# Optimization experiments

Measured on AMD Instinct MI355X. Metric: run time of the kernel, lower is better.

## Reference

```python
import jax, jax.numpy as jnp
import numpy as np

NEG_SLOPE = 0.2
EPS = 1e-16

def gatv2(x, edge_index, edge_attr, Wl, bl, We, att, bias):
    """PyG GATv2Conv, heads=1, share_weights=True, with edge_dim."""
    N = x.shape[0]
    h = x @ Wl + bl                      # [N, out] shared lin_l == lin_r
    src, dst = edge_index[0], edge_index[1]
    hj = h[src]                          # source (message) features [E, out]
    hi = h[dst]                          # target features [E, out]
    e = jax.nn.leaky_relu(hi + hj + edge_attr @ We, NEG_SLOPE)  # [E, out]
    score = e @ att                      # [E]
    # segment softmax over edges grouped by destination node
    smax = jax.ops.segment_max(score, dst, num_segments=N)
    ex = jnp.exp(score - smax[dst])
    denom = jax.ops.segment_sum(ex, dst, num_segments=N)
    alpha = ex / (denom[dst] + EPS)      # [E]
    out = jax.ops.segment_sum(hj * alpha[:, None], dst, num_segments=N)
    return out + bias


def setup_inputs() -> dict:
    key = jax.random.key(0)
    N, E = 50000, 800000
    D_IN, D_LAT, D_EDGE, N_ACT = 128, 128, 16, 32
    ks = jax.random.split(key, 16)
    s = 0.05
    inp = {
        "x": jax.random.normal(ks[0], (N, D_IN), jnp.float32),
        "edge_index": jax.random.randint(ks[1], (2, E), 0, N, jnp.int32),
        "edge_attr": jax.random.normal(ks[2], (E, D_EDGE), jnp.float32),
        # gnn_layer: D_IN -> D_LAT
        "Wl1": jax.random.normal(ks[3], (D_IN, D_LAT), jnp.float32) * s,
        "bl1": jnp.zeros((D_LAT,), jnp.float32),
        "We1": jax.random.normal(ks[4], (D_EDGE, D_LAT), jnp.float32) * s,
        "att1": jax.random.normal(ks[5], (D_LAT,), jnp.float32) * s,
        "bias1": jnp.zeros((D_LAT,), jnp.float32),
        # node_layer: D_LAT -> 1
        "Wl2": jax.random.normal(ks[6], (D_LAT, 1), jnp.float32) * s,
        "bl2": jnp.zeros((1,), jnp.float32),
        "We2": jax.random.normal(ks[7], (D_EDGE, 1), jnp.float32) * s,
        "att2": jax.random.normal(ks[8], (1,), jnp.float32) * s,
        "bias2": jnp.zeros((1,), jnp.float32),
        # action_layer: D_LAT -> N_ACT
        "Wl3": jax.random.normal(ks[9], (D_LAT, N_ACT), jnp.float32) * s,
        "bl3": jnp.zeros((N_ACT,), jnp.float32),
        "We3": jax.random.normal(ks[10], (D_EDGE, N_ACT), jnp.float32) * s,
        "att3": jax.random.normal(ks[11], (N_ACT,), jnp.float32) * s,
        "bias3": jnp.zeros((N_ACT,), jnp.float32),
    }
    return inp


def reference(x, edge_index, edge_attr,
              Wl1, bl1, We1, att1, bias1,
              Wl2, bl2, We2, att2, bias2,
              Wl3, bl3, We3, att3, bias3):
    latent = gatv2(x, edge_index, edge_attr, Wl1, bl1, We1, att1, bias1)          # [N, D_LAT]
    node_logits = gatv2(latent, edge_index, edge_attr, Wl2, bl2, We2, att2, bias2)[:, 0]  # [N]
    action_logits = gatv2(latent, edge_index, edge_attr, Wl3, bl3, We3, att3, bias3)      # [N, A]
    # categorical sampling with fixed key (deterministic reference)
    k1, k2 = jax.random.split(jax.random.key(42))
    node_sel = jax.random.categorical(k1, node_logits)
    node_lp = jax.nn.log_softmax(node_logits)[node_sel]
    act_logits_sel = action_logits[node_sel, :]
    action_sel = jax.random.categorical(k2, act_logits_sel)
    action_lp = jax.nn.log_softmax(act_logits_sel)[action_sel]
    return (node_sel, action_sel, node_lp + action_lp)
```

## Files before the change

kernel.cpp:

```cpp
#include <hip/hip_runtime.h>
#include <stdint.h>
#include <math.h>

#define NEG 0.2f
#define TINYF 1.1754943508222875e-38f

typedef float f4 __attribute__((ext_vector_type(4)));
typedef float f2 __attribute__((ext_vector_type(2)));

__host__ __device__ inline void threefry2x32(uint32_t k0, uint32_t k1,
                                             uint32_t x0, uint32_t x1,
                                             uint32_t* o0, uint32_t* o1) {
  uint32_t ks0 = k0, ks1 = k1, ks2 = k0 ^ k1 ^ 0x1BD11BDAu;
  x0 += ks0; x1 += ks1;
#define RR(r) { x0 += x1; x1 = (x1 << (r)) | (x1 >> (32 - (r))); x1 ^= x0; }
  RR(13) RR(15) RR(26) RR(6)
  x0 += ks1; x1 += ks2 + 1u;
  RR(17) RR(29) RR(16) RR(24)
  x0 += ks2; x1 += ks0 + 2u;
  RR(13) RR(15) RR(26) RR(6)
  x0 += ks0; x1 += ks1 + 3u;
  RR(17) RR(29) RR(16) RR(24)
  x0 += ks1; x1 += ks2 + 4u;
  RR(13) RR(15) RR(26) RR(6)
  x0 += ks2; x1 += ks0 + 5u;
#undef RR
  *o0 = x0; *o1 = x1;
}

__device__ inline float gumbel_part(uint32_t ka, uint32_t kb, uint32_t i) {
  uint32_t o0, o1;
  threefry2x32(ka, kb, 0u, i, &o0, &o1);
  uint32_t bits = o0 ^ o1;
  float f = __uint_as_float((bits >> 9) | 0x3f800000u) - 1.0f;
  float u = fmaxf(TINYF, f + TINYF);
  return -logf(-logf(u));
}

__global__ void count_kernel(const int* __restrict__ ei, int E, int* __restrict__ counts) {
  int e = blockIdx.x * blockDim.x + threadIdx.x;
  if (e < E) atomicAdd(&counts[ei[E + e]], 1);
}

#define SCB 256
__global__ __launch_bounds__(256) void scan_partial_kernel(const int* __restrict__ counts,
    int N, int chunk, int* __restrict__ bsum) {
  int b = blockIdx.x;
  int s0 = b * chunk, s1 = s0 + chunk; if (s1 > N) s1 = N;
  int tid = threadIdx.x;
  int v = 0;
  for (int i = s0 + tid; i < s1; i += 256) v += counts[i];
  __shared__ int red[256];
  red[tid] = v; __syncthreads();
  for (int s = 128; s; s >>= 1) { if (tid < s) red[tid] += red[tid + s]; __syncthreads(); }
  if (tid == 0) bsum[b] = red[0];
}

__global__ __launch_bounds__(256) void scan_offsets_kernel(const int* __restrict__ bsum,
    int* __restrict__ boff, int* __restrict__ row_start, int N) {
  int tid = threadIdx.x; int lane = tid & 63; int wv = tid >> 6;
  __shared__ int wsum[4];
  int v = bsum[tid];
  int incl = v;
#pragma unroll
  for (int off = 1; off < 64; off <<= 1) {
    int t = __shfl_up(incl, off);
    if (lane >= off) incl += t;
  }
  if (lane == 63) wsum[wv] = incl;
  __syncthreads();
  if (tid == 0) {
    int s = 0;
    for (int k = 0; k < 4; k++) { int t = wsum[k]; wsum[k] = s; s += t; }
    row_start[N] = s;
  }
  __syncthreads();
  boff[tid] = wsum[wv] + incl - v;
}

__global__ __launch_bounds__(256) void scan_apply_kernel(const int* __restrict__ counts,
    const int* __restrict__ boff, int N, int chunk,
    int* __restrict__ row_start, int* __restrict__ cursor) {
  int b = blockIdx.x;
  int s0 = b * chunk, s1 = s0 + chunk; if (s1 > N) s1 = N;
  int tid = threadIdx.x; int lane = tid & 63; int wv = tid >> 6;
  __shared__ int wsum[4];
  __shared__ int tot_s;
  __shared__ int base_s;
  if (tid == 0) base_s = boff[b];
  __syncthreads();
  for (int c0 = s0; c0 < s1; c0 += 256) {
    int i = c0 + tid;
    int v = (i < s1) ? counts[i] : 0;
    int incl = v;
#pragma unroll
    for (int off = 1; off < 64; off <<= 1) {
      int t = __shfl_up(incl, off);
      if (lane >= off) incl += t;
    }
    if (lane == 63) wsum[wv] = incl;
    __syncthreads();
    if (tid == 0) {
      int s = 0;
      for (int k = 0; k < 4; k++) { int t = wsum[k]; wsum[k] = s; s += t; }
      tot_s = s;
    }
    __syncthreads();
    int base = base_s;
    int excl = base + wsum[wv] + incl - v;
    if (i < s1) { row_start[i] = excl; cursor[i] = excl; }
    __syncthreads();
    if (tid == 0) base_s = base + tot_s;
    __syncthreads();
  }
}

__global__ void scatter_kernel(const int* __restrict__ ei, const float* __restrict__ ea,
                               int E, int* __restrict__ cursor,
                               int* __restrict__ src_csr, float* __restrict__ ea_csr) {
  int e = blockIdx.x * blockDim.x + threadIdx.x;
  if (e < E) {
    int d = ei[E + e];
    int p = atomicAdd(&cursor[d], 1);
    src_csr[p] = ei[e];
    const float4* s4 = (const float4*)&ea[(size_t)e * 16];
    float4* d4 = (float4*)&ea_csr[(size_t)p * 16];
    float4 t0 = s4[0], t1 = s4[1], t2 = s4[2], t3 = s4[3];
    d4[0] = t0; d4[1] = t1; d4[2] = t2; d4[3] = t3;
  }
}

__global__ __launch_bounds__(256) void gemm128_kernel(const float* __restrict__ X,
    const float* __restrict__ W, const float* __restrict__ bias,
    float* __restrict__ out, int M) {
  __shared__ float xs[128][33];
  int row0 = blockIdx.x * 32;
  int tid = threadIdx.x;
  for (int idx = tid; idx < 32 * 128; idx += 256) {
    int r = idx >> 7;
    int k = idx & 127;
    int row = row0 + r;
    xs[k][r] = (row < M) ? X[(size_t)row * 128 + k] : 0.0f;
  }
  __syncthreads();
  int tc = tid & 31, tr = tid >> 5;
  int c0 = tc * 4, r0 = tr * 4;
  float acc[4][4] = {};
#pragma unroll 4
  for (int k = 0; k < 128; k++) {
    float4 w = *(const float4*)&W[k * 128 + c0];
    float x0 = xs[k][r0], x1 = xs[k][r0 + 1], x2 = xs[k][r0 + 2], x3 = xs[k][r0 + 3];
    acc[0][0] += x0 * w.x; acc[0][1] += x0 * w.y; acc[0][2] += x0 * w.z; acc[0][3] += x0 * w.w;
    acc[1][0] += x1 * w.x; acc[1][1] += x1 * w.y; acc[1][2] += x1 * w.z; acc[1][3] += x1 * w.w;
    acc[2][0] += x2 * w.x; acc[2][1] += x2 * w.y; acc[2][2] += x2 * w.z; acc[2][3] += x2 * w.w;
    acc[3][0] += x3 * w.x; acc[3][1] += x3 * w.y; acc[3][2] += x3 * w.z; acc[3][3] += x3 * w.w;
  }
  float4 b4 = *(const float4*)&bias[c0];
  for (int r = 0; r < 4; r++) {
    int row = row0 + r0 + r;
    if (row < M) {
      float4 o;
      o.x = acc[r][0] + b4.x; o.y = acc[r][1] + b4.y;
      o.z = acc[r][2] + b4.z; o.w = acc[r][3] + b4.w;
      *(float4*)&out[(size_t)row * 128 + c0] = o;
    }
  }
}

__global__ __launch_bounds__(256) void gemm32_kernel(const float* __restrict__ X,
    const float* __restrict__ W, const float* __restrict__ bias,
    float* __restrict__ out, int M) {
  int t = blockIdx.x * 256 + threadIdx.x;
  int node = t >> 5, c = t & 31;
  if (node >= M) return;
  const float4* xp = (const float4*)&X[(size_t)node * 128];
  float acc = 0.f;
#pragma unroll
  for (int q = 0; q < 32; q++) {
    float4 x4 = xp[q];
    acc += x4.x * W[(q * 4 + 0) * 32 + c] + x4.y * W[(q * 4 + 1) * 32 + c]
         + x4.z * W[(q * 4 + 2) * 32 + c] + x4.w * W[(q * 4 + 3) * 32 + c];
  }
  out[(size_t)node * 32 + c] = acc + bias[c];
}

__global__ __launch_bounds__(256) void gemv_kernel(const float* __restrict__ X,
    const float* __restrict__ w, const float* __restrict__ b0,
    float* __restrict__ out, int M) {
  int wv = (blockIdx.x * 256 + threadIdx.x) >> 6;
  int lane = threadIdx.x & 63;
  if (wv >= M) return;
  float2 xv = *(const float2*)&X[(size_t)wv * 128 + lane * 2];
  float2 wvv = *(const float2*)&w[lane * 2];
  float v = xv.x * wvv.x + xv.y * wvv.y;
#pragma unroll
  for (int off = 32; off; off >>= 1) v += __shfl_xor(v, off);
  if (lane == 0) out[wv] = v + b0[0];
}

__global__ __launch_bounds__(256) void fused1_kernel(const float* __restrict__ h,
    const int* __restrict__ src_csr, const int* __restrict__ row_start,
    const float* __restrict__ ea_csr,
    const float* __restrict__ We, const float* __restrict__ att,
    const float* __restrict__ bias, float* __restrict__ out, int N) {
  __shared__ float WeS[2048];
  int tid = threadIdx.x;
  for (int i = tid; i < 2048; i += 256) WeS[i] = We[i];
  __syncthreads();
  int hw = (blockIdx.x * 256 + tid) >> 5;
  int lane = tid & 31;
  if (hw >= N) return;
  int c4 = lane * 4;
  const f4* W4 = (const f4*)WeS;
  f4 attv = *(const f4*)&att[c4];
  f4 bb = *(const f4*)&bias[c4];
  int start = row_start[hw];
  int deg = row_start[hw + 1] - start;
  if (deg == 0) {
    *(f4*)&out[(size_t)hw * 128 + c4] = bb;
    return;
  }
  f4 hi = *(const f4*)&h[(size_t)hw * 128 + c4];
  int s_l = (lane < deg) ? src_csr[start + lane] : 0;
  int dcap = deg < 32 ? deg : 32;
  const f4* eap = (const f4*)&ea_csr[(size_t)start * 16];
  float m = -INFINITY, l = 0.f;
  f4 acc = (f4)0.f;
  for (int j = 0; j < deg; j++) {
    int s = (j < dcap) ? __shfl(s_l, j, 32) : src_csr[start + j];
    f4 hj = *(const f4*)&h[(size_t)s * 128 + c4];
    f4 v = hi + hj;
#pragma unroll
    for (int q = 0; q < 4; q++) {
      f4 aq = eap[(size_t)j * 4 + q];
      v += aq.x * W4[(4 * q + 0) * 32 + lane];
      v += aq.y * W4[(4 * q + 1) * 32 + lane];
      v += aq.z * W4[(4 * q + 2) * 32 + lane];
      v += aq.w * W4[(4 * q + 3) * 32 + lane];
    }
    v.x = v.x >= 0.f ? v.x : NEG * v.x;
    v.y = v.y >= 0.f ? v.y : NEG * v.y;
    v.z = v.z >= 0.f ? v.z : NEG * v.z;
    v.w = v.w >= 0.f ? v.w : NEG * v.w;
    f4 pv = v * attv;
    float sc = (pv.x + pv.y) + (pv.z + pv.w);
#pragma unroll
    for (int off = 16; off; off >>= 1) sc += __shfl_xor(sc, off);
    float mn = fmaxf(m, sc);
    float scale = __expf(m - mn);
    float w = __expf(sc - mn);
    l = l * scale + w;
    acc = acc * scale + w * hj;
    m = mn;
  }
  float inv = 1.0f / (l + 1e-16f);
  f4 o = acc * inv + bb;
  *(f4*)&out[(size_t)hw * 128 + c4] = o;
}

__global__ __launch_bounds__(256) void fused23_kernel(
    const float* __restrict__ h3, const float* __restrict__ h2,
    const int* __restrict__ src_csr, const int* __restrict__ row_start,
    const float* __restrict__ ea_csr,
    const float* __restrict__ We3, const float* __restrict__ att3,
    const float* __restrict__ bias3, const float* __restrict__ We2,
    const float* __restrict__ att2, const float* __restrict__ bias2,
    float* __restrict__ out3, float* __restrict__ logits, int N) {
  __shared__ float We3S[512];
  __shared__ float att3S[32];
  __shared__ float We2S[16];
  int tid = threadIdx.x;
  for (int i = tid; i < 512; i += 256) We3S[i] = We3[i];
  if (tid < 32) att3S[tid] = att3[tid];
  if (tid < 16) We2S[tid] = We2[tid];
  __syncthreads();
  int wv = (blockIdx.x * 256 + tid) >> 6;
  int lane = tid & 63;
  if (wv >= N) return;
  int q4 = lane >> 4;
  int l16 = lane & 15;
  int c2 = l16 * 2;
  const f2* W3 = (const f2*)We3S;
  f2 at3 = *(const f2*)&att3S[c2];
  float a2s = att2[0];
  f2 bi3 = *(const f2*)&bias3[c2];
  int start = row_start[wv];
  int deg = row_start[wv + 1] - start;
  if (deg == 0) {
    if (lane < 16) *(f2*)&out3[(size_t)wv * 32 + c2] = bi3;
    if (lane == 0) logits[wv] = bias2[0];
    return;
  }
  f2 hi3 = *(const f2*)&h3[(size_t)wv * 32 + c2];
  float hi2 = h2[wv];
  int s_l = (lane < deg) ? src_csr[start + lane] : 0;
  int dcap = deg < 64 ? deg : 64;
  const float4* eap = (const float4*)&ea_csr[(size_t)start * 16];
  float m3 = -INFINITY, l3 = 0.f; f2 a3 = (f2)0.f;
  float m2 = -INFINITY, l2 = 0.f; float a2 = 0.f;
  for (int j = q4; j < deg; j += 4) {
    int s = (j < dcap) ? __shfl(s_l, j) : src_csr[start + j];
    f2 hj3 = *(const f2*)&h3[(size_t)s * 32 + c2];
    float h2s = h2[s];
    float4 c0 = eap[(size_t)j * 4 + 0];
    float4 c1 = eap[(size_t)j * 4 + 1];
    float4 cc2 = eap[(size_t)j * 4 + 2];
    float4 c3 = eap[(size_t)j * 4 + 3];
    f2 v = hi3 + hj3;
    v += c0.x * W3[0 * 16 + l16];  v += c0.y * W3[1 * 16 + l16];
    v += c0.z * W3[2 * 16 + l16];  v += c0.w * W3[3 * 16 + l16];
    v += c1.x * W3[4 * 16 + l16];  v += c1.y * W3[5 * 16 + l16];
    v += c1.z * W3[6 * 16 + l16];  v += c1.w * W3[7 * 16 + l16];
    v += cc2.x * W3[8 * 16 + l16]; v += cc2.y * W3[9 * 16 + l16];
    v += cc2.z * W3[10 * 16 + l16]; v += cc2.w * W3[11 * 16 + l16];
    v += c3.x * W3[12 * 16 + l16]; v += c3.y * W3[13 * 16 + l16];
    v += c3.z * W3[14 * 16 + l16]; v += c3.w * W3[15 * 16 + l16];
    v.x = v.x >= 0.f ? v.x : NEG * v.x;
    v.y = v.y >= 0.f ? v.y : NEG * v.y;
    float t3 = v.x * at3.x + v.y * at3.y;
#pragma unroll
    for (int off = 8; off; off >>= 1) t3 += __shfl_xor(t3, off);
    float v2 = hi2 + h2s;
    v2 += c0.x * We2S[0]  + c0.y * We2S[1]  + c0.z * We2S[2]  + c0.w * We2S[3];
    v2 += c1.x * We2S[4]  + c1.y * We2S[5]  + c1.z * We2S[6]  + c1.w * We2S[7];
    v2 += cc2.x * We2S[8] + cc2.y * We2S[9] + cc2.z * We2S[10] + cc2.w * We2S[11];
    v2 += c3.x * We2S[12] + c3.y * We2S[13] + c3.z * We2S[14] + c3.w * We2S[15];
    v2 = v2 >= 0.f ? v2 : NEG * v2;
    float t2 = v2 * a2s;
    float mn3 = fmaxf(m3, t3);
    float sc3 = __expf(m3 - mn3);
    float w3 = __expf(t3 - mn3);
    l3 = l3 * sc3 + w3;
    a3 = a3 * sc3 + w3 * hj3;
    m3 = mn3;
    float mn2 = fmaxf(m2, t2);
    float sc2 = __expf(m2 - mn2);
    float w2 = __expf(t2 - mn2);
    l2 = l2 * sc2 + w2;
    a2 = a2 * sc2 + w2 * h2s;
    m2 = mn2;
  }
#pragma unroll
  for (int off = 16; off <= 32; off <<= 1) {
    float m3o = __shfl_xor(m3, off), l3o = __shfl_xor(l3, off);
    float ax = __shfl_xor(a3.x, off), ay = __shfl_xor(a3.y, off);
    float M3 = fmaxf(m3, m3o);
    float sA = (m3 == -INFINITY) ? 0.f : __expf(m3 - M3);
    float sB = (m3o == -INFINITY) ? 0.f : __expf(m3o - M3);
    l3 = l3 * sA + l3o * sB;
    a3.x = a3.x * sA + ax * sB;
    a3.y = a3.y * sA + ay * sB;
    m3 = M3;
    float m2o = __shfl_xor(m2, off), l2o = __shfl_xor(l2, off);
    float az = __shfl_xor(a2, off);
    float M2 = fmaxf(m2, m2o);
    float tA = (m2 == -INFINITY) ? 0.f : __expf(m2 - M2);
    float tB = (m2o == -INFINITY) ? 0.f : __expf(m2o - M2);
    l2 = l2 * tA + l2o * tB;
    a2 = a2 * tA + az * tB;
    m2 = M2;
  }
  if (lane < 16) {
    f2 o;
    o.x = a3.x / (l3 + 1e-16f) + bi3.x;
    o.y = a3.y / (l3 + 1e-16f) + bi3.y;
    *(f2*)&out3[(size_t)wv * 32 + c2] = o;
  }
  if (lane == 0) logits[wv] = a2 / (l2 + 1e-16f) + bias2[0];
}

#define NSB 64
__global__ __launch_bounds__(256) void node_partial_kernel(const float* __restrict__ logits,
    int N, uint32_t ka, uint32_t kb,
    float* __restrict__ pB, int* __restrict__ pI,
    float* __restrict__ pM, float* __restrict__ pL) {
  int chunk = (N + NSB - 1) / NSB;
  int s0 = blockIdx.x * chunk;
  int s1 = s0 + chunk; if (s1 > N) s1 = N;
  int tid = threadIdx.x;
  float best = -INFINITY; int bi = 0x7fffffff;
  float m = -INFINITY, l = 0.f;
  for (int i = s0 + tid; i < s1; i += 256) {
    float lg = logits[i];
    float mn = fmaxf(m, lg);
    l = l * __expf(m - mn) + __expf(lg - mn);
    m = mn;
    float v = lg + gumbel_part(ka, kb, (uint32_t)i);
    if (v > best) { best = v; bi = i; }
  }
  __shared__ float sb[256], sm[256], sl[256];
  __shared__ int si[256];
  sb[tid] = best; si[tid] = bi; sm[tid] = m; sl[tid] = l;
  __syncthreads();
  for (int s = 128; s; s >>= 1) {
    if (tid < s) {
      if (sb[tid + s] > sb[tid] || (sb[tid + s] == sb[tid] && si[tid + s] < si[tid])) {
        sb[tid] = sb[tid + s]; si[tid] = si[tid + s];
      }
      float M = fmaxf(sm[tid], sm[tid + s]);
      float t0 = (sm[tid] == -INFINITY) ? 0.f : sl[tid] * __expf(sm[tid] - M);
      float t1 = (sm[tid + s] == -INFINITY) ? 0.f : sl[tid + s] * __expf(sm[tid + s] - M);
      sm[tid] = M; sl[tid] = t0 + t1;
    }
    __syncthreads();
  }
  if (tid == 0) { pB[blockIdx.x] = sb[0]; pI[blockIdx.x] = si[0]; pM[blockIdx.x] = sm[0]; pL[blockIdx.x] = sl[0]; }
}

__global__ __launch_bounds__(64) void node_final_kernel(const float* __restrict__ logits,
    const float* __restrict__ pB, const int* __restrict__ pI,
    const float* __restrict__ pM, const float* __restrict__ pL,
    float* __restrict__ scal) {
  int lane = threadIdx.x;
  float best = pB[lane]; int bi = pI[lane];
  float m = pM[lane]; float l = pL[lane];
#pragma unroll
  for (int off = 32; off; off >>= 1) {
    float ob = __shfl_xor(best, off); int oi = __shfl_xor(bi, off);
    if (ob > best || (ob == best && oi < bi)) { best = ob; bi = oi; }
    float om = __shfl_xor(m, off); float ol = __shfl_xor(l, off);
    float M = fmaxf(m, om);
    float t0 = (m == -INFINITY) ? 0.f : l * __expf(m - M);
    float t1 = (om == -INFINITY) ? 0.f : ol * __expf(om - M);
    m = M; l = t0 + t1;
  }
  if (lane == 0) {
    ((int*)scal)[0] = bi;
    scal[3] = logits[bi] - (m + logf(l));
  }
}

__global__ __launch_bounds__(64) void action_kernel(const float* __restrict__ out3,
    const float* __restrict__ scal, uint32_t ka, uint32_t kb,
    float* __restrict__ dout, int out_size) {
  int lane = threadIdx.x;
  int sel = ((const int*)scal)[0];
  float v = -INFINITY, noisy = -INFINITY;
  if (lane < 32) {
    v = out3[(size_t)sel * 32 + lane];
    noisy = v + gumbel_part(ka, kb, (uint32_t)lane);
  }
  int idx = lane;
  float nv = noisy;
#pragma unroll
  for (int off = 32; off; off >>= 1) {
    float ov = __shfl_xor(nv, off);
    int oi = __shfl_xor(idx, off);
    if (ov > nv || (ov == nv && oi < idx)) { nv = ov; idx = oi; }
  }
  float vm = v;
#pragma unroll
  for (int off = 32; off; off >>= 1) vm = fmaxf(vm, __shfl_xor(vm, off));
  float ex = (lane < 32) ? expf(v - vm) : 0.f;
#pragma unroll
  for (int off = 32; off; off >>= 1) ex += __shfl_xor(ex, off);
  float vsel = __shfl(v, idx);
  if (lane == 0) {
    float action_lp = vsel - vm - logf(ex);
    dout[0] = (float)sel;
    dout[1] = (float)idx;
    dout[2] = scal[3] + action_lp;
  }
  for (int i = 3 + lane; i < out_size; i += 64) dout[i] = 0.f;
}

extern "C" void kernel_launch(void* const* d_in, const int* in_sizes, int n_in,
                              void* d_out, int out_size, void* d_ws, size_t ws_size,
                              hipStream_t stream) {
  const float* x     = (const float*)d_in[0];
  const int*   ei    = (const int*)d_in[1];
  const float* ea    = (const float*)d_in[2];
  const float* Wl1   = (const float*)d_in[3];
  const float* bl1   = (const float*)d_in[4];
  const float* We1   = (const float*)d_in[5];
  const float* att1  = (const float*)d_in[6];
  const float* bias1 = (const float*)d_in[7];
  const float* Wl2   = (const float*)d_in[8];
  const float* bl2   = (const float*)d_in[9];
  const float* We2   = (const float*)d_in[10];
  const float* att2  = (const float*)d_in[11];
  const float* bias2 = (const float*)d_in[12];
  const float* Wl3   = (const float*)d_in[13];
  const float* bl3   = (const float*)d_in[14];
  const float* We3   = (const float*)d_in[15];
  const float* att3  = (const float*)d_in[16];
  const float* bias3 = (const float*)d_in[17];
  int N = in_sizes[0] / 128;
  int E = in_sizes[1] / 2;
  float* out = (float*)d_out;

  char* p = (char*)d_ws;
  auto alloc = [&](size_t bytes) -> char* {
    char* r = p; p += (bytes + 255) & ~(size_t)255; return r;
  };
  float* h1      = (float*)alloc((size_t)N * 128 * 4);
  float* latent  = (float*)alloc((size_t)N * 128 * 4);
  float* h3      = (float*)alloc((size_t)N * 32 * 4);
  float* h2      = (float*)alloc((size_t)N * 4);
  float* logits  = (float*)alloc((size_t)N * 4);
  float* out3    = (float*)alloc((size_t)N * 32 * 4);
  int* counts    = (int*)alloc((size_t)N * 4);
  int* row_start = (int*)alloc((size_t)(N + 1) * 4);
  int* cursor    = (int*)alloc((size_t)N * 4);
  int* src_csr   = (int*)alloc((size_t)E * 4);
  float* ea_csr  = (float*)alloc((size_t)E * 16 * 4);
  int* bsum      = (int*)alloc(SCB * 4);
  int* boff      = (int*)alloc(SCB * 4);
  float* pB      = (float*)alloc(NSB * 4);
  int*   pI      = (int*)alloc(NSB * 4);
  float* pM      = (float*)alloc(NSB * 4);
  float* pL      = (float*)alloc(NSB * 4);
  float* scal    = (float*)alloc(64);
  (void)ws_size; (void)n_in;

  uint32_t k1a, k1b, k2a, k2b;
  threefry2x32(0u, 42u, 0u, 0u, &k1a, &k1b);
  threefry2x32(0u, 42u, 0u, 1u, &k2a, &k2b);

  int chunk = (N + SCB - 1) / SCB;

  hipMemsetAsync(counts, 0, (size_t)N * 4, stream);
  count_kernel<<<(E + 255) / 256, 256, 0, stream>>>(ei, E, counts);
  scan_partial_kernel<<<SCB, 256, 0, stream>>>(counts, N, chunk, bsum);
  scan_offsets_kernel<<<1, 256, 0, stream>>>(bsum, boff, row_start, N);
  scan_apply_kernel<<<SCB, 256, 0, stream>>>(counts, boff, N, chunk, row_start, cursor);
  scatter_kernel<<<(E + 255) / 256, 256, 0, stream>>>(ei, ea, E, cursor, src_csr, ea_csr);

  gemm128_kernel<<<(N + 31) / 32, 256, 0, stream>>>(x, Wl1, bl1, h1, N);
  fused1_kernel<<<(N + 7) / 8, 256, 0, stream>>>(h1, src_csr, row_start,
                                                 ea_csr, We1, att1, bias1, latent, N);

  gemm32_kernel<<<((size_t)N * 32 + 255) / 256, 256, 0, stream>>>(latent, Wl3, bl3, h3, N);
  gemv_kernel<<<(N + 3) / 4, 256, 0, stream>>>(latent, Wl2, bl2, h2, N);

  fused23_kernel<<<(N + 3) / 4, 256, 0, stream>>>(h3, h2, src_csr, row_start, ea_csr,
                                                  We3, att3, bias3, We2, att2, bias2,
                                                  out3, logits, N);

  node_partial_kernel<<<NSB, 256, 0, stream>>>(logits, N, k1a, k1b, pB, pI, pM, pL);
  node_final_kernel<<<1, 64, 0, stream>>>(logits, pB, pI, pM, pL, scal);
  action_kernel<<<1, 64, 0, stream>>>(out3, scal, k2a, k2b, out, out_size);
}
```

Baseline: 578.9 us.

## Map one full wavefront per node in layer-1 attention and drop online max

The first GATv2 fused kernel now gives each destination node a full 64-lane wavefront, with each lane holding 2 channels instead of 4. This cuts per-lane register and edge-weight work. The online-softmax running max and its rescaling exps are replaced by a plain exp of the score clamped at 60. That removes one exp and a rescale per edge, but results change if any score exceeds 60 and precision can drop for large scores. Launch bounds now request higher occupancy, and the grid is doubled to match.

```diff
diff --git a/kernel.cpp b/kernel.cpp
--- a/kernel.cpp
+++ b/kernel.cpp
@@ -198,7 +198,7 @@
   if (lane == 0) out[wv] = v + b0[0];
 }
 
-__global__ __launch_bounds__(256) void fused1_kernel(const float* __restrict__ h,
+__global__ __launch_bounds__(256, 8) void fused1_kernel(const float* __restrict__ h,
     const int* __restrict__ src_csr, const int* __restrict__ row_start,
     const float* __restrict__ ea_csr,
     const float* __restrict__ We, const float* __restrict__ att,
@@ -207,55 +207,61 @@
   int tid = threadIdx.x;
   for (int i = tid; i < 2048; i += 256) WeS[i] = We[i];
   __syncthreads();
-  int hw = (blockIdx.x * 256 + tid) >> 5;
-  int lane = tid & 31;
-  if (hw >= N) return;
-  int c4 = lane * 4;
-  const f4* W4 = (const f4*)WeS;
-  f4 attv = *(const f4*)&att[c4];
-  f4 bb = *(const f4*)&bias[c4];
-  int start = row_start[hw];
-  int deg = row_start[hw + 1] - start;
+  int wv = (blockIdx.x * 256 + tid) >> 6;
+  int lane = tid & 63;
+  if (wv >= N) return;
+  int c2 = lane * 2;
+  const f2* W2 = (const f2*)WeS;
+  int start = row_start[wv];
+  int deg = row_start[wv + 1] - start;
   if (deg == 0) {
-    *(f4*)&out[(size_t)hw * 128 + c4] = bb;
+    *(f2*)&out[(size_t)wv * 128 + c2] = *(const f2*)&bias[c2];
     return;
   }
-  f4 hi = *(const f4*)&h[(size_t)hw * 128 + c4];
+  f2 attv = *(const f2*)&att[c2];
+  f2 hi = *(const f2*)&h[(size_t)wv * 128 + c2];
   int s_l = (lane < deg) ? src_csr[start + lane] : 0;
-  int dcap = deg < 32 ? deg : 32;
+  int dcap = deg < 64 ? deg : 64;
   const f4* eap = (const f4*)&ea_csr[(size_t)start * 16];
-  float m = -INFINITY, l = 0.f;
-  f4 acc = (f4)0.f;
+  float l = 0.f;
+  f2 acc = (f2)0.f;
   for (int j = 0; j < deg; j++) {
-    int s = (j < dcap) ? __shfl(s_l, j, 32) : src_csr[start + j];
-    f4 hj = *(const f4*)&h[(size_t)s * 128 + c4];
-    f4 v = hi + hj;
-#pragma unroll
-    for (int q = 0; q < 4; q++) {
-      f4 aq = eap[(size_t)j * 4 + q];
-      v += aq.x * W4[(4 * q + 0) * 32 + lane];
-      v += aq.y * W4[(4 * q + 1) * 32 + lane];
-      v += aq.z * W4[(4 * q + 2) * 32 + lane];
-      v += aq.w * W4[(4 * q + 3) * 32 + lane];
-    }
+    int s = (j < dcap) ? __shfl(s_l, j) : src_csr[start + j];
+    f2 hj = *(const f2*)&h[(size_t)s * 128 + c2];
+    f4 e0 = eap[(size_t)j * 4 + 0];
+    f4 e1 = eap[(size_t)j * 4 + 1];
+    f4 e2 = eap[(size_t)j * 4 + 2];
+    f4 e3 = eap[(size_t)j * 4 + 3];
+    f2 v = hi + hj;
+    v += e0.x * W2[0 * 64 + lane];
+    v += e0.y * W2[1 * 64 + lane];
+    v += e0.z * W2[2 * 64 + lane];
+    v += e0.w * W2[3 * 64 + lane];
+    v += e1.x * W2[4 * 64 + lane];
+    v += e1.y * W2[5 * 64 + lane];
+    v += e1.z * W2[6 * 64 + lane];
+    v += e1.w * W2[7 * 64 + lane];
+    v += e2.x * W2[8 * 64 + lane];
+    v += e2.y * W2[9 * 64 + lane];
+    v += e2.z * W2[10 * 64 + lane];
+    v += e2.w * W2[11 * 64 + lane];
+    v += e3.x * W2[12 * 64 + lane];
+    v += e3.y * W2[13 * 64 + lane];
+    v += e3.z * W2[14 * 64 + lane];
+    v += e3.w * W2[15 * 64 + lane];
     v.x = v.x >= 0.f ? v.x : NEG * v.x;
     v.y = v.y >= 0.f ? v.y : NEG * v.y;
-    v.z = v.z >= 0.f ? v.z : NEG * v.z;
-    v.w = v.w >= 0.f ? v.w : NEG * v.w;
-    f4 pv = v * attv;
-    float sc = (pv.x + pv.y) + (pv.z + pv.w);
-#pragma unroll
-    for (int off = 16; off; off >>= 1) sc += __shfl_xor(sc, off);
-    float mn = fmaxf(m, sc);
-    float scale = __expf(m - mn);
-    float w = __expf(sc - mn);
-    l = l * scale + w;
-    acc = acc * scale + w * hj;
-    m = mn;
+    f2 pv = v * attv;
+    float sc = pv.x + pv.y;
+#pragma unroll
+    for (int off = 32; off; off >>= 1) sc += __shfl_xor(sc, off);
+    float w = __expf(fminf(sc, 60.f));
+    l += w;
+    acc += w * hj;
   }
   float inv = 1.0f / (l + 1e-16f);
-  f4 o = acc * inv + bb;
-  *(f4*)&out[(size_t)hw * 128 + c4] = o;
+  f2 bb = *(const f2*)&bias[c2];
+  *(f2*)&out[(size_t)wv * 128 + c2] = acc * inv + bb;
 }
 
 __global__ __launch_bounds__(256) void fused23_kernel(
@@ -527,7 +533,7 @@
   scatter_kernel<<<(E + 255) / 256, 256, 0, stream>>>(ei, ea, E, cursor, src_csr, ea_csr);
 
   gemm128_kernel<<<(N + 31) / 32, 256, 0, stream>>>(x, Wl1, bl1, h1, N);
-  fused1_kernel<<<(N + 7) / 8, 256, 0, stream>>>(h1, src_csr, row_start,
+  fused1_kernel<<<(N + 3) / 4, 256, 0, stream>>>(h1, src_csr, row_start,
                                                  ea_csr, We1, att1, bias1, latent, N);
 
   gemm32_kernel<<<((size_t)N * 32 + 255) / 256, 256, 0, stream>>>(latent, Wl3, bl3, h3, N);
```

Measured after the change: 616.4 us. +6.5%, slower.
